# Kernel optimization log

Hardware: AMD Instinct MI355X
Metric: run time of the kernel (lower is better)

## Reference

```python
import jax, jax.numpy as jnp
import numpy as np

H = 8  # num_heads
EPS = 1e-5


def layer_norm(x, g, b):
    mu = jnp.mean(x, axis=-1, keepdims=True)
    var = jnp.mean((x - mu) ** 2, axis=-1, keepdims=True)
    return (x - mu) * jax.lax.rsqrt(var + EPS) * g + b


def setup_inputs() -> dict:
    key = jax.random.key(0)
    ks = jax.random.split(key, 8)
    B, N, C = 2, 2048, 512
    Dff = 2048
    s = 0.02
    x = jax.random.normal(ks[0], (B, N, C), dtype=jnp.float32)
    mask = (jax.random.uniform(ks[1], (N, N)) > 0.5).astype(jnp.float32)
    return {
        "x": x,
        "mask": mask,
        "w_qkv": jax.random.normal(ks[2], (3 * C, C), dtype=jnp.float32) * s,
        "w_proj": jax.random.normal(ks[3], (C, C), dtype=jnp.float32) * s,
        "b_proj": jnp.zeros((C,), jnp.float32),
        "g1": jnp.ones((C,), jnp.float32),
        "beta1": jnp.zeros((C,), jnp.float32),
        "g2": jnp.ones((C,), jnp.float32),
        "beta2": jnp.zeros((C,), jnp.float32),
        "w1": jax.random.normal(ks[4], (Dff, C), dtype=jnp.float32) * s,
        "bm1": jnp.zeros((Dff,), jnp.float32),
        "w2": jax.random.normal(ks[5], (C, Dff), dtype=jnp.float32) * s,
        "bm2": jnp.zeros((C,), jnp.float32),
    }


def attn_block(h, mask, w_qkv, w_proj, b_proj):
    B, N, C = h.shape
    hd = C // H
    scale = hd ** -0.5
    qkv = (h @ w_qkv.T).reshape(B, N, 3, H, hd)
    q, k, v = jnp.moveaxis(qkv, 2, 0)          # each [B, N, H, hd]
    q = q.transpose(0, 2, 1, 3)                 # [B, H, N, hd]
    k = k.transpose(0, 2, 1, 3)
    v = v.transpose(0, 2, 1, 3)
    attn = jnp.einsum("bhnd,bhmd->bhnm", q, k) * scale
    attn = attn * mask                          # multiplicative sparse mask
    attn = jax.nn.softmax(attn, axis=-1)
    o = jnp.einsum("bhnm,bhmd->bhnd", attn, v)
    o = o.transpose(0, 2, 1, 3).reshape(B, N, C)
    return o @ w_proj.T + b_proj


def reference(x, mask, w_qkv, w_proj, b_proj, g1, beta1, g2, beta2, w1, bm1, w2, bm2):
    # pre-norm transformer block, dropout/drop_path disabled (eval)
    y = x + attn_block(layer_norm(x, g1, beta1), mask, w_qkv, w_proj, b_proj)
    h = layer_norm(y, g2, beta2)
    h = jax.nn.gelu(h @ w1.T + bm1, approximate=False)  # torch F.gelu default (erf)
    z = y + (h @ w2.T + bm2)
    return z
```

## Files before the change

### kernel.cpp

```cpp
#include <hip/hip_runtime.h>
#include <cmath>
#include <stdint.h>

#define N_SEQ 2048
#define C_DIM 512
#define BATCH 2
#define NHEAD 8
#define DFF   2048
#define M_ROWS (BATCH * N_SEQ)

typedef unsigned short ushort_t;
typedef __bf16 bf16x8 __attribute__((ext_vector_type(8)));
typedef float  f32x4  __attribute__((ext_vector_type(4)));

__device__ __forceinline__ float bf2f(ushort_t u) {
    union { unsigned int i; float f; } v; v.i = ((unsigned int)u) << 16; return v.f;
}
__device__ __forceinline__ ushort_t f2bf_(float f) {
    union { float f; unsigned int i; } v; v.f = f;
    unsigned int r = v.i + 0x7fffu + ((v.i >> 16) & 1u);
    return (ushort_t)(r >> 16);
}

__device__ __forceinline__ void load_lds16(const ushort_t* g, ushort_t* lds_wave_base) {
    __builtin_amdgcn_global_load_lds(
        (const __attribute__((address_space(1))) void*)g,
        (__attribute__((address_space(3))) void*)lds_wave_base, 16, 0, 0);
}

__global__ void probe_kernel(const unsigned int* __restrict__ g1w, int* __restrict__ flag) {
    if (threadIdx.x == 0 && blockIdx.x == 0)
        *flag = (g1w[0] == 0x3F800000u) ? 1 : 0;
}

__global__ __launch_bounds__(256) void convert_kernel(const int* __restrict__ flag,
        const void* w_qkv, const void* w_proj, const void* w1, const void* w2,
        ushort_t* wq_bf, ushort_t* wp_bf, ushort_t* w1_bf, ushort_t* w2_bf) {
    long e = ((long)blockIdx.x * 256 + threadIdx.x) * 8;
    const void* src; ushort_t* dst; long off;
    if      (e < 786432)  { src = w_qkv; dst = wq_bf;  off = e; }
    else if (e < 1048576) { src = w_proj; dst = wp_bf; off = e - 786432; }
    else if (e < 2097152) { src = w1;    dst = w1_bf;  off = e - 1048576; }
    else                  { src = w2;    dst = w2_bf;  off = e - 2097152; }
    bf16x8 r;
    if (*flag) {
        const float4* q = (const float4*)((const float*)src + off);
        float4 a = q[0], b = q[1];
        r[0]=(__bf16)a.x; r[1]=(__bf16)a.y; r[2]=(__bf16)a.z; r[3]=(__bf16)a.w;
        r[4]=(__bf16)b.x; r[5]=(__bf16)b.y; r[6]=(__bf16)b.z; r[7]=(__bf16)b.w;
    } else {
        r = *(const bf16x8*)((const ushort_t*)src + off);
    }
    *(bf16x8*)(dst + off) = r;
}

template <typename TX, typename TG>
__device__ __forceinline__ void ln_body(const TX* __restrict__ x, const TG* __restrict__ g,
                                        const TG* __restrict__ b, ushort_t* __restrict__ out) {
    int row  = blockIdx.x * 4 + (threadIdx.x >> 6);
    int lane = threadIdx.x & 63;
    const TX* xr = x + (size_t)row * C_DIM + lane * 8;
    float v[8];
    if (sizeof(TX) == 2) {
        bf16x8 t = *(const bf16x8*)xr;
        #pragma unroll
        for (int j = 0; j < 8; ++j) v[j] = (float)t[j];
    } else {
        const float4* q = (const float4*)xr;
        float4 a = q[0], c = q[1];
        v[0]=a.x; v[1]=a.y; v[2]=a.z; v[3]=a.w; v[4]=c.x; v[5]=c.y; v[6]=c.z; v[7]=c.w;
    }
    float s = 0.f, sq = 0.f;
    #pragma unroll
    for (int j = 0; j < 8; ++j) { s += v[j]; sq += v[j] * v[j]; }
    #pragma unroll
    for (int m = 1; m < 64; m <<= 1) { s += __shfl_xor(s, m, 64); sq += __shfl_xor(sq, m, 64); }
    float mean = s * (1.0f / C_DIM);
    float var  = fmaxf(sq * (1.0f / C_DIM) - mean * mean, 0.0f);
    float rs = rsqrtf(var + 1e-5f);
    float gv[8], bv[8];
    const TG* gp = g + lane * 8; const TG* bp = b + lane * 8;
    if (sizeof(TG) == 2) {
        bf16x8 tg = *(const bf16x8*)gp, tb = *(const bf16x8*)bp;
        #pragma unroll
        for (int j = 0; j < 8; ++j) { gv[j] = (float)tg[j]; bv[j] = (float)tb[j]; }
    } else {
        const float4* qg = (const float4*)gp; const float4* qb = (const float4*)bp;
        float4 a=qg[0], c=qg[1], d=qb[0], e=qb[1];
        gv[0]=a.x;gv[1]=a.y;gv[2]=a.z;gv[3]=a.w;gv[4]=c.x;gv[5]=c.y;gv[6]=c.z;gv[7]=c.w;
        bv[0]=d.x;bv[1]=d.y;bv[2]=d.z;bv[3]=d.w;bv[4]=e.x;bv[5]=e.y;bv[6]=e.z;bv[7]=e.w;
    }
    bf16x8 o;
    #pragma unroll
    for (int j = 0; j < 8; ++j) o[j] = (__bf16)((v[j] - mean) * rs * gv[j] + bv[j]);
    *(bf16x8*)(out + (size_t)row * C_DIM + lane * 8) = o;
}

__global__ __launch_bounds__(256) void ln1_kernel(const int* __restrict__ flag, const void* x,
                                                  const void* g, const void* b, ushort_t* out) {
    if (*flag) ln_body<float, float>((const float*)x, (const float*)g, (const float*)b, out);
    else       ln_body<ushort_t, ushort_t>((const ushort_t*)x, (const ushort_t*)g, (const ushort_t*)b, out);
}
__global__ __launch_bounds__(256) void ln2_kernel(const int* __restrict__ flag, const ushort_t* y,
                                                  const void* g, const void* b, ushort_t* out) {
    if (*flag) ln_body<ushort_t, float>(y, (const float*)g, (const float*)b, out);
    else       ln_body<ushort_t, ushort_t>(y, (const ushort_t*)g, (const ushort_t*)b, out);
}

template <int BM, int K, bool HAS_BIAS, int ACT, int RES_MODE, int OUT_MODE>
__global__ __launch_bounds__(256) void gemm_kernel(const int* __restrict__ flag,
        const ushort_t* __restrict__ A, const ushort_t* __restrict__ W,
        const void* __restrict__ bias, const void* __restrict__ res,
        void* __restrict__ Cout, int Nout) {
    constexpr int MT = BM / 32;
    __shared__ __align__(16) ushort_t As[BM * 32];
    __shared__ __align__(16) ushort_t Bs[64 * 32];
    int t = threadIdx.x;
    int wave = t >> 6, lane = t & 63, quad = lane >> 4, l16 = lane & 15;
    int wave_m = wave >> 1, wave_n = wave & 1;
    int row0 = blockIdx.y * BM, col0 = blockIdx.x * 64;

    f32x4 acc[MT][2] = {};
    int arow = t >> 2, kofs = (t & 3) * 8;

    for (int k0 = 0; k0 < K; k0 += 32) {
        load_lds16(A + (size_t)(row0 + arow) * K + k0 + kofs, As + wave * 512);
        if (BM == 128)
            load_lds16(A + (size_t)(row0 + 64 + arow) * K + k0 + kofs, As + 2048 + wave * 512);
        load_lds16(W + (size_t)(col0 + arow) * K + k0 + kofs, Bs + wave * 512);
        __syncthreads();
        bf16x8 af[MT], bfr[2];
        #pragma unroll
        for (int i = 0; i < MT; ++i)
            af[i] = *(const bf16x8*)&As[(wave_m * (BM / 2) + i * 16 + l16) * 32 + quad * 8];
        #pragma unroll
        for (int j = 0; j < 2; ++j)
            bfr[j] = *(const bf16x8*)&Bs[(wave_n * 32 + j * 16 + l16) * 32 + quad * 8];
        #pragma unroll
        for (int i = 0; i < MT; ++i)
            #pragma unroll
            for (int j = 0; j < 2; ++j)
                acc[i][j] = __builtin_amdgcn_mfma_f32_16x16x32_bf16(af[i], bfr[j], acc[i][j], 0, 0, 0);
        __syncthreads();
    }

    int is32 = *flag;
    #pragma unroll
    for (int j = 0; j < 2; ++j) {
        int col = col0 + wave_n * 32 + j * 16 + l16;
        float bv = 0.0f;
        if (HAS_BIAS) bv = is32 ? ((const float*)bias)[col] : bf2f(((const ushort_t*)bias)[col]);
        #pragma unroll
        for (int i = 0; i < MT; ++i) {
            #pragma unroll
            for (int r = 0; r < 4; ++r) {
                int row = row0 + wave_m * (BM / 2) + i * 16 + quad * 4 + r;
                float v = acc[i][j][r] + bv;
                if (ACT == 1) v = 0.5f * v * (1.0f + erff(v * 0.70710678118654752f));
                size_t idx = (size_t)row * Nout + col;
                if (RES_MODE == 1) v += is32 ? ((const float*)res)[idx] : bf2f(((const ushort_t*)res)[idx]);
                if (RES_MODE == 3) v += bf2f(((const ushort_t*)res)[idx]);
                if (OUT_MODE == 0) ((ushort_t*)Cout)[idx] = f2bf_(v);
                else { if (is32) ((float*)Cout)[idx] = v; else ((ushort_t*)Cout)[idx] = f2bf_(v); }
            }
        }
    }
}

__global__ __launch_bounds__(256, 5) void attn_kernel(const int* __restrict__ flag,
        const ushort_t* __restrict__ qkv, const void* __restrict__ mask,
        ushort_t* __restrict__ Opart, float* __restrict__ Lpart) {
    __shared__ __align__(16) ushort_t Ks[64][68];
    __shared__ __align__(16) ushort_t VTs[64][68];
    __shared__ __align__(16) ushort_t Ps[4][16][68];
    int bh = blockIdx.x, b = bh >> 3, h = bh & 7;
    int sp = blockIdx.z;
    int t = threadIdx.x;
    int wave = t >> 6, lane = t & 63, quad = lane >> 4, l16 = lane & 15;
    int row0 = blockIdx.y * 64 + wave * 16;
    int is32 = *flag;

    const ushort_t* base = qkv + (size_t)b * N_SEQ * 1536;
    const ushort_t* qp = base + h * 64;
    const ushort_t* kp = base + 512 + h * 64;
    const ushort_t* vp = base + 1024 + h * 64;
    const float* mask32 = (const float*)mask;
    const ushort_t* mask16 = (const ushort_t*)mask;
    size_t mbase[4];
    #pragma unroll
    for (int r = 0; r < 4; ++r) mbase[r] = (size_t)(row0 + quad * 4 + r) * N_SEQ;

    bf16x8 aq[2];
    #pragma unroll
    for (int c = 0; c < 2; ++c)
        aq[c] = *(const bf16x8*)(qp + (size_t)(row0 + l16) * 1536 + c * 32 + quad * 8);

    f32x4 o_acc[4] = {};
    float lsum[4] = {};
    const float scale = 0.125f;

    int k_key[2], k_d[2], v_key[2], v_db[2];
    #pragma unroll
    for (int s = 0; s < 2; ++s) {
        int e = s * 256 + t;
        k_key[s] = e >> 3;  k_d[s]  = (e & 7) * 8;
        v_key[s] = e & 63;  v_db[s] = (e >> 6) * 8;
    }
    const int n_base = sp * 512;
    bf16x8 kreg[2], vreg[2];
    #pragma unroll
    for (int s = 0; s < 2; ++s) {
        kreg[s] = *(const bf16x8*)(kp + (size_t)(n_base + k_key[s]) * 1536 + k_d[s]);
        vreg[s] = *(const bf16x8*)(vp + (size_t)(n_base + v_key[s]) * 1536 + v_db[s]);
    }
    float mreg[16];
    #pragma unroll
    for (int g = 0; g < 4; ++g)
        #pragma unroll
        for (int r = 0; r < 4; ++r) {
            size_t midx = mbase[r] + n_base + g * 16 + l16;
            mreg[g * 4 + r] = is32 ? mask32[midx] : bf2f(mask16[midx]);
        }

    for (int i = 0; i < 8; ++i) {
        int n0 = n_base + i * 64;
        __syncthreads();
        #pragma unroll
        for (int s = 0; s < 2; ++s)
            *(bf16x8*)&Ks[k_key[s]][k_d[s]] = kreg[s];
        #pragma unroll
        for (int s = 0; s < 2; ++s)
            #pragma unroll
            for (int j = 0; j < 8; ++j)
                VTs[v_db[s] + j][v_key[s]] = __builtin_bit_cast(unsigned short, vreg[s][j]);
        __syncthreads();
        if (i < 7) {
            int n1 = n0 + 64;
            #pragma unroll
            for (int s = 0; s < 2; ++s) {
                kreg[s] = *(const bf16x8*)(kp + (size_t)(n1 + k_key[s]) * 1536 + k_d[s]);
                vreg[s] = *(const bf16x8*)(vp + (size_t)(n1 + v_key[s]) * 1536 + v_db[s]);
            }
        }
        f32x4 s_acc[4] = {};
        #pragma unroll
        for (int g = 0; g < 4; ++g)
            #pragma unroll
            for (int c = 0; c < 2; ++c) {
                bf16x8 bk = *(const bf16x8*)&Ks[g * 16 + l16][c * 32 + quad * 8];
                s_acc[g] = __builtin_amdgcn_mfma_f32_16x16x32_bf16(aq[c], bk, s_acc[g], 0, 0, 0);
            }
        #pragma unroll
        for (int g = 0; g < 4; ++g)
            #pragma unroll
            for (int r = 0; r < 4; ++r) {
                float p = __expf(s_acc[g][r] * scale * mreg[g * 4 + r]);
                lsum[r] += p;
                Ps[wave][quad * 4 + r][g * 16 + l16] = __builtin_bit_cast(unsigned short, (__bf16)p);
            }
        if (i < 7) {
            #pragma unroll
            for (int g = 0; g < 4; ++g)
                #pragma unroll
                for (int r = 0; r < 4; ++r) {
                    size_t midx = mbase[r] + n0 + 64 + g * 16 + l16;
                    mreg[g * 4 + r] = is32 ? mask32[midx] : bf2f(mask16[midx]);
                }
        }
        bf16x8 pf[2];
        #pragma unroll
        for (int c = 0; c < 2; ++c)
            pf[c] = *(const bf16x8*)&Ps[wave][l16][c * 32 + quad * 8];
        #pragma unroll
        for (int d = 0; d < 4; ++d)
            #pragma unroll
            for (int c = 0; c < 2; ++c) {
                bf16x8 bv = *(const bf16x8*)&VTs[d * 16 + l16][c * 32 + quad * 8];
                o_acc[d] = __builtin_amdgcn_mfma_f32_16x16x32_bf16(pf[c], bv, o_acc[d], 0, 0, 0);
            }
    }
    #pragma unroll
    for (int m = 1; m < 16; m <<= 1)
        #pragma unroll
        for (int r = 0; r < 4; ++r) lsum[r] += __shfl_xor(lsum[r], m, 64);
    ushort_t* op = Opart + (size_t)(sp * 16 + bh) * N_SEQ * 64;
    #pragma unroll
    for (int r = 0; r < 4; ++r) {
        int row = row0 + quad * 4 + r;
        #pragma unroll
        for (int d = 0; d < 4; ++d)
            op[(size_t)row * 64 + d * 16 + l16] = f2bf_(o_acc[d][r]);
    }
    if (l16 == 0) {
        #pragma unroll
        for (int r = 0; r < 4; ++r)
            Lpart[(size_t)(sp * 16 + bh) * N_SEQ + row0 + quad * 4 + r] = lsum[r];
    }
}

__global__ __launch_bounds__(256) void combine_kernel(const ushort_t* __restrict__ Opart,
        const float* __restrict__ Lpart, ushort_t* __restrict__ attno) {
    int gid = blockIdx.x * 256 + threadIdx.x;
    int rowg = gid >> 4;
    int dq = (gid & 15) * 4;
    int bh = rowg >> 11, q = rowg & 2047, b = bh >> 3, h = bh & 7;
    const size_t SP = (size_t)16 * N_SEQ * 64;
    float acc[4] = {};
    float l = 0.0f;
    #pragma unroll
    for (int sp = 0; sp < 4; ++sp) {
        ushort4 o = *(const ushort4*)&Opart[sp * SP + (size_t)rowg * 64 + dq];
        acc[0] += bf2f(o.x); acc[1] += bf2f(o.y); acc[2] += bf2f(o.z); acc[3] += bf2f(o.w);
        l += Lpart[(size_t)sp * 16 * N_SEQ + rowg];
    }
    float inv = 1.0f / l;
    ushort4 res;
    res.x = f2bf_(acc[0] * inv); res.y = f2bf_(acc[1] * inv);
    res.z = f2bf_(acc[2] * inv); res.w = f2bf_(acc[3] * inv);
    *(ushort4*)&attno[((size_t)b * N_SEQ + q) * C_DIM + h * 64 + dq] = res;
}

extern "C" void kernel_launch(void* const* d_in, const int* in_sizes, int n_in,
                              void* d_out, int out_size, void* d_ws, size_t ws_size,
                              hipStream_t stream) {
    char* ws = (char*)d_ws;
    const size_t KB = 1024;
    int*      flag  = (int*)ws;
    ushort_t* wq_bf = (ushort_t*)(ws + 256 * KB);
    ushort_t* wp_bf = (ushort_t*)(ws + 1792 * KB);
    ushort_t* w1_bf = (ushort_t*)(ws + 2304 * KB);
    ushort_t* w2_bf = (ushort_t*)(ws + 4352 * KB);
    ushort_t* h     = (ushort_t*)(ws + 6400 * KB);
    ushort_t* attno = (ushort_t*)(ws + 6400 * KB);
    ushort_t* qkv   = (ushort_t*)(ws + 10496 * KB);
    ushort_t* Opart = (ushort_t*)(ws + 22784 * KB);
    float*    Lpart = (float*)   (ws + 39168 * KB);
    ushort_t* y     = (ushort_t*)(ws + 35072 * KB);
    ushort_t* gmid  = (ushort_t*)(ws + 10496 * KB);

    probe_kernel<<<1, 64, 0, stream>>>((const unsigned int*)d_in[5], flag);
    convert_kernel<<<1536, 256, 0, stream>>>(flag, d_in[2], d_in[3], d_in[9], d_in[11],
                                             wq_bf, wp_bf, w1_bf, w2_bf);
    ln1_kernel<<<M_ROWS / 4, 256, 0, stream>>>(flag, d_in[0], d_in[5], d_in[6], h);
    gemm_kernel<128, 512, false, 0, 0, 0><<<dim3(1536 / 64, 32), 256, 0, stream>>>(
        flag, h, wq_bf, nullptr, nullptr, qkv, 1536);
    attn_kernel<<<dim3(BATCH * NHEAD, N_SEQ / 64, 4), 256, 0, stream>>>(flag, qkv, d_in[1], Opart, Lpart);
    combine_kernel<<<2048, 256, 0, stream>>>(Opart, Lpart, attno);
    gemm_kernel<64, 512, true, 0, 1, 0><<<dim3(C_DIM / 64, 64), 256, 0, stream>>>(
        flag, attno, wp_bf, d_in[4], d_in[0], y, C_DIM);
    ln2_kernel<<<M_ROWS / 4, 256, 0, stream>>>(flag, y, d_in[7], d_in[8], h);
    gemm_kernel<128, 512, true, 1, 0, 0><<<dim3(DFF / 64, 32), 256, 0, stream>>>(
        flag, h, w1_bf, d_in[10], nullptr, gmid, DFF);
    gemm_kernel<64, 2048, true, 0, 3, 2><<<dim3(C_DIM / 64, 64), 256, 0, stream>>>(
        flag, gmid, w2_bf, d_in[12], y, d_out, C_DIM);
}
```

Before: 275.9 us.

## Pack mask to bits, switch attention to 32x32 MFMA, double GEMM k-step

```diff
diff --git a/kernel.cpp b/kernel.cpp
--- a/kernel.cpp
+++ b/kernel.cpp
@@ -10,8 +10,10 @@
 #define M_ROWS (BATCH * N_SEQ)
 
 typedef unsigned short ushort_t;
+typedef unsigned long long u64;
 typedef __bf16 bf16x8 __attribute__((ext_vector_type(8)));
 typedef float  f32x4  __attribute__((ext_vector_type(4)));
+typedef float  f32x16 __attribute__((ext_vector_type(16)));
 
 __device__ __forceinline__ float bf2f(ushort_t u) {
     union { unsigned int i; float f; } v; v.i = ((unsigned int)u) << 16; return v.f;
@@ -54,6 +56,20 @@
     *(bf16x8*)(dst + off) = r;
 }
 
+__global__ __launch_bounds__(256) void maskpack_kernel(const int* __restrict__ flag,
+        const void* __restrict__ mask, u64* __restrict__ maskT) {
+    int key = blockIdx.x * 256 + threadIdx.x;
+    int qw  = blockIdx.y;
+    int is32 = *flag;
+    u64 bits = 0;
+    for (int j = 0; j < 64; ++j) {
+        bool m = is32 ? (((const float*)mask)[(size_t)(qw * 64 + j) * N_SEQ + key] != 0.0f)
+                      : ((((const ushort_t*)mask)[(size_t)(qw * 64 + j) * N_SEQ + key] & 0x7fffu) != 0);
+        bits |= (u64)m << j;
+    }
+    maskT[(size_t)key * 32 + qw] = bits;
+}
+
 template <typename TX, typename TG>
 __device__ __forceinline__ void ln_body(const TX* __restrict__ x, const TG* __restrict__ g,
                                         const TG* __restrict__ b, ushort_t* __restrict__ out) {
@@ -113,8 +129,8 @@
         const void* __restrict__ bias, const void* __restrict__ res,
         void* __restrict__ Cout, int Nout) {
     constexpr int MT = BM / 32;
-    __shared__ __align__(16) ushort_t As[BM * 32];
-    __shared__ __align__(16) ushort_t Bs[64 * 32];
+    __shared__ __align__(16) ushort_t As[2][BM][32];
+    __shared__ __align__(16) ushort_t Bs[2][64][32];
     int t = threadIdx.x;
     int wave = t >> 6, lane = t & 63, quad = lane >> 4, l16 = lane & 15;
     int wave_m = wave >> 1, wave_n = wave & 1;
@@ -123,24 +139,30 @@
     f32x4 acc[MT][2] = {};
     int arow = t >> 2, kofs = (t & 3) * 8;
 
-    for (int k0 = 0; k0 < K; k0 += 32) {
-        load_lds16(A + (size_t)(row0 + arow) * K + k0 + kofs, As + wave * 512);
-        if (BM == 128)
-            load_lds16(A + (size_t)(row0 + 64 + arow) * K + k0 + kofs, As + 2048 + wave * 512);
-        load_lds16(W + (size_t)(col0 + arow) * K + k0 + kofs, Bs + wave * 512);
+    for (int k0 = 0; k0 < K; k0 += 64) {
+        #pragma unroll
+        for (int h = 0; h < 2; ++h) {
+            load_lds16(A + (size_t)(row0 + arow) * K + k0 + h * 32 + kofs, &As[h][0][0] + wave * 512);
+            if (BM == 128)
+                load_lds16(A + (size_t)(row0 + 64 + arow) * K + k0 + h * 32 + kofs, &As[h][64][0] + wave * 512);
+            load_lds16(W + (size_t)(col0 + arow) * K + k0 + h * 32 + kofs, &Bs[h][0][0] + wave * 512);
+        }
         __syncthreads();
-        bf16x8 af[MT], bfr[2];
-        #pragma unroll
-        for (int i = 0; i < MT; ++i)
-            af[i] = *(const bf16x8*)&As[(wave_m * (BM / 2) + i * 16 + l16) * 32 + quad * 8];
-        #pragma unroll
-        for (int j = 0; j < 2; ++j)
-            bfr[j] = *(const bf16x8*)&Bs[(wave_n * 32 + j * 16 + l16) * 32 + quad * 8];
-        #pragma unroll
-        for (int i = 0; i < MT; ++i)
+        #pragma unroll
+        for (int h = 0; h < 2; ++h) {
+            bf16x8 af[MT], bfr[2];
+            #pragma unroll
+            for (int i = 0; i < MT; ++i)
+                af[i] = *(const bf16x8*)&As[h][wave_m * (BM / 2) + i * 16 + l16][quad * 8];
             #pragma unroll
             for (int j = 0; j < 2; ++j)
-                acc[i][j] = __builtin_amdgcn_mfma_f32_16x16x32_bf16(af[i], bfr[j], acc[i][j], 0, 0, 0);
+                bfr[j] = *(const bf16x8*)&Bs[h][wave_n * 32 + j * 16 + l16][quad * 8];
+            #pragma unroll
+            for (int i = 0; i < MT; ++i)
+                #pragma unroll
+                for (int j = 0; j < 2; ++j)
+                    acc[i][j] = __builtin_amdgcn_mfma_f32_16x16x32_bf16(af[i], bfr[j], acc[i][j], 0, 0, 0);
+        }
         __syncthreads();
     }
 
@@ -167,134 +189,125 @@
     }
 }
 
-__global__ __launch_bounds__(256, 5) void attn_kernel(const int* __restrict__ flag,
-        const ushort_t* __restrict__ qkv, const void* __restrict__ mask,
+__global__ __launch_bounds__(128, 3) void attn_kernel(const int* __restrict__ flag,
+        const ushort_t* __restrict__ qkv, const u64* __restrict__ maskT,
         ushort_t* __restrict__ Opart, float* __restrict__ Lpart) {
-    __shared__ __align__(16) ushort_t Ks[64][68];
+    __shared__ __align__(16) ushort_t Ks[64][64];
     __shared__ __align__(16) ushort_t VTs[64][68];
-    __shared__ __align__(16) ushort_t Ps[4][16][68];
-    int bh = blockIdx.x, b = bh >> 3, h = bh & 7;
-    int sp = blockIdx.z;
+    __shared__ __align__(16) ushort_t Ps[2][32][68];
     int t = threadIdx.x;
-    int wave = t >> 6, lane = t & 63, quad = lane >> 4, l16 = lane & 15;
-    int row0 = blockIdx.y * 64 + wave * 16;
-    int is32 = *flag;
+    int wave = t >> 6, lane = t & 63, l32 = lane & 31, half = lane >> 5;
+    int qtile = blockIdx.x, bh = blockIdx.y, sp = blockIdx.z;
+    int b = bh >> 3, h = bh & 7;
+    int qbase = qtile * 64;
 
     const ushort_t* base = qkv + (size_t)b * N_SEQ * 1536;
     const ushort_t* qp = base + h * 64;
     const ushort_t* kp = base + 512 + h * 64;
     const ushort_t* vp = base + 1024 + h * 64;
-    const float* mask32 = (const float*)mask;
-    const ushort_t* mask16 = (const ushort_t*)mask;
-    size_t mbase[4];
-    #pragma unroll
-    for (int r = 0; r < 4; ++r) mbase[r] = (size_t)(row0 + quad * 4 + r) * N_SEQ;
-
-    bf16x8 aq[2];
-    #pragma unroll
-    for (int c = 0; c < 2; ++c)
-        aq[c] = *(const bf16x8*)(qp + (size_t)(row0 + l16) * 1536 + c * 32 + quad * 8);
-
-    f32x4 o_acc[4] = {};
-    float lsum[4] = {};
+
+    bf16x8 aq[4];
+    int qrow = qbase + wave * 32 + l32;
+    #pragma unroll
+    for (int c = 0; c < 4; ++c)
+        aq[c] = *(const bf16x8*)(qp + (size_t)qrow * 1536 + c * 16 + half * 8);
+
+    f32x16 o_acc[2] = {};
+    float lsum[16] = {};
     const float scale = 0.125f;
 
-    int k_key[2], k_d[2], v_key[2], v_db[2];
+    int v_kp[2], v_db[2];
     #pragma unroll
     for (int s = 0; s < 2; ++s) {
-        int e = s * 256 + t;
-        k_key[s] = e >> 3;  k_d[s]  = (e & 7) * 8;
-        v_key[s] = e & 63;  v_db[s] = (e >> 6) * 8;
+        int idx = s * 128 + t;
+        v_kp[s] = (idx & 31) * 2;
+        v_db[s] = (idx >> 5) * 8;
     }
     const int n_base = sp * 512;
-    bf16x8 kreg[2], vreg[2];
-    #pragma unroll
-    for (int s = 0; s < 2; ++s) {
-        kreg[s] = *(const bf16x8*)(kp + (size_t)(n_base + k_key[s]) * 1536 + k_d[s]);
-        vreg[s] = *(const bf16x8*)(vp + (size_t)(n_base + v_key[s]) * 1536 + v_db[s]);
-    }
-    float mreg[16];
-    #pragma unroll
-    for (int g = 0; g < 4; ++g)
-        #pragma unroll
-        for (int r = 0; r < 4; ++r) {
-            size_t midx = mbase[r] + n_base + g * 16 + l16;
-            mreg[g * 4 + r] = is32 ? mask32[midx] : bf2f(mask16[midx]);
-        }
+    bf16x8 vreg[2][2];
+    #pragma unroll
+    for (int s = 0; s < 2; ++s)
+        #pragma unroll
+        for (int u = 0; u < 2; ++u)
+            vreg[s][u] = *(const bf16x8*)(vp + (size_t)(n_base + v_kp[s] + u) * 1536 + v_db[s]);
+    u64 mw[2];
+    #pragma unroll
+    for (int t2 = 0; t2 < 2; ++t2)
+        mw[t2] = maskT[(size_t)(n_base + t2 * 32 + l32) * 32 + qtile];
 
     for (int i = 0; i < 8; ++i) {
         int n0 = n_base + i * 64;
         __syncthreads();
         #pragma unroll
+        for (int s = 0; s < 4; ++s)
+            load_lds16(kp + (size_t)(n0 + (s * 2 + wave) * 8 + (lane >> 3)) * 1536 + (lane & 7) * 8,
+                       &Ks[(s * 2 + wave) * 8][0]);
+        #pragma unroll
         for (int s = 0; s < 2; ++s)
-            *(bf16x8*)&Ks[k_key[s]][k_d[s]] = kreg[s];
-        #pragma unroll
-        for (int s = 0; s < 2; ++s)
-            #pragma unroll
-            for (int j = 0; j < 8; ++j)
-                VTs[v_db[s] + j][v_key[s]] = __builtin_bit_cast(unsigned short, vreg[s][j]);
+            #pragma unroll
+            for (int j = 0; j < 8; ++j) {
+                unsigned int pair = (unsigned int)__builtin_bit_cast(unsigned short, vreg[s][0][j])
+                                  | ((unsigned int)__builtin_bit_cast(unsigned short, vreg[s][1][j]) << 16);
+                *(unsigned int*)&VTs[v_db[s] + j][v_kp[s]] = pair;
+            }
         __syncthreads();
         if (i < 7) {
             int n1 = n0 + 64;
             #pragma unroll
-            for (int s = 0; s < 2; ++s) {
-                kreg[s] = *(const bf16x8*)(kp + (size_t)(n1 + k_key[s]) * 1536 + k_d[s]);
-                vreg[s] = *(const bf16x8*)(vp + (size_t)(n1 + v_key[s]) * 1536 + v_db[s]);
-            }
-        }
-        f32x4 s_acc[4] = {};
-        #pragma unroll
-        for (int g = 0; g < 4; ++g)
-            #pragma unroll
-            for (int c = 0; c < 2; ++c) {
-                bf16x8 bk = *(const bf16x8*)&Ks[g * 16 + l16][c * 32 + quad * 8];
-                s_acc[g] = __builtin_amdgcn_mfma_f32_16x16x32_bf16(aq[c], bk, s_acc[g], 0, 0, 0);
-            }
-        #pragma unroll
-        for (int g = 0; g < 4; ++g)
-            #pragma unroll
-            for (int r = 0; r < 4; ++r) {
-                float p = __expf(s_acc[g][r] * scale * mreg[g * 4 + r]);
+            for (int s = 0; s < 2; ++s)
+                #pragma unroll
+                for (int u = 0; u < 2; ++u)
+                    vreg[s][u] = *(const bf16x8*)(vp + (size_t)(n1 + v_kp[s] + u) * 1536 + v_db[s]);
+        }
+        f32x16 s_acc[2] = {};
+        #pragma unroll
+        for (int t2 = 0; t2 < 2; ++t2)
+            #pragma unroll
+            for (int c = 0; c < 4; ++c) {
+                bf16x8 bk = *(const bf16x8*)&Ks[t2 * 32 + l32][c * 16 + half * 8];
+                s_acc[t2] = __builtin_amdgcn_mfma_f32_32x32x16_bf16(aq[c], bk, s_acc[t2], 0, 0, 0);
+            }
+        #pragma unroll
+        for (int t2 = 0; t2 < 2; ++t2)
+            #pragma unroll
+            for (int r = 0; r < 16; ++r) {
+                int row_local = (r & 3) + 8 * (r >> 2) + 4 * half;
+                float e = __expf(s_acc[t2][r] * scale);
+                float p = ((mw[t2] >> (wave * 32 + row_local)) & 1) ? e : 1.0f;
                 lsum[r] += p;
-                Ps[wave][quad * 4 + r][g * 16 + l16] = __builtin_bit_cast(unsigned short, (__bf16)p);
+                Ps[wave][row_local][t2 * 32 + l32] = __builtin_bit_cast(unsigned short, (__bf16)p);
             }
         if (i < 7) {
             #pragma unroll
-            for (int g = 0; g < 4; ++g)
-                #pragma unroll
-                for (int r = 0; r < 4; ++r) {
-                    size_t midx = mbase[r] + n0 + 64 + g * 16 + l16;
-                    mreg[g * 4 + r] = is32 ? mask32[midx] : bf2f(mask16[midx]);
-                }
-        }
-        bf16x8 pf[2];
-        #pragma unroll
-        for (int c = 0; c < 2; ++c)
-            pf[c] = *(const bf16x8*)&Ps[wave][l16][c * 32 + quad * 8];
-        #pragma unroll
-        for (int d = 0; d < 4; ++d)
-            #pragma unroll
-            for (int c = 0; c < 2; ++c) {
-                bf16x8 bv = *(const bf16x8*)&VTs[d * 16 + l16][c * 32 + quad * 8];
-                o_acc[d] = __builtin_amdgcn_mfma_f32_16x16x32_bf16(pf[c], bv, o_acc[d], 0, 0, 0);
-            }
-    }
-    #pragma unroll
-    for (int m = 1; m < 16; m <<= 1)
-        #pragma unroll
-        for (int r = 0; r < 4; ++r) lsum[r] += __shfl_xor(lsum[r], m, 64);
+            for (int t2 = 0; t2 < 2; ++t2)
+                mw[t2] = maskT[(size_t)(n0 + 64 + t2 * 32 + l32) * 32 + qtile];
+        }
+        bf16x8 pf[4];
+        #pragma unroll
+        for (int kc = 0; kc < 4; ++kc)
+            pf[kc] = *(const bf16x8*)&Ps[wave][l32][kc * 16 + half * 8];
+        #pragma unroll
+        for (int dt = 0; dt < 2; ++dt)
+            #pragma unroll
+            for (int kc = 0; kc < 4; ++kc) {
+                bf16x8 bv = *(const bf16x8*)&VTs[dt * 32 + l32][kc * 16 + half * 8];
+                o_acc[dt] = __builtin_amdgcn_mfma_f32_32x32x16_bf16(pf[kc], bv, o_acc[dt], 0, 0, 0);
+            }
+    }
+    #pragma unroll
+    for (int m = 1; m < 32; m <<= 1)
+        #pragma unroll
+        for (int r = 0; r < 16; ++r) lsum[r] += __shfl_xor(lsum[r], m, 64);
     ushort_t* op = Opart + (size_t)(sp * 16 + bh) * N_SEQ * 64;
     #pragma unroll
-    for (int r = 0; r < 4; ++r) {
-        int row = row0 + quad * 4 + r;
-        #pragma unroll
-        for (int d = 0; d < 4; ++d)
-            op[(size_t)row * 64 + d * 16 + l16] = f2bf_(o_acc[d][r]);
-    }
-    if (l16 == 0) {
-        #pragma unroll
-        for (int r = 0; r < 4; ++r)
-            Lpart[(size_t)(sp * 16 + bh) * N_SEQ + row0 + quad * 4 + r] = lsum[r];
+    for (int r = 0; r < 16; ++r) {
+        int row_local = (r & 3) + 8 * (r >> 2) + 4 * half;
+        int q = qbase + wave * 32 + row_local;
+        #pragma unroll
+        for (int dt = 0; dt < 2; ++dt)
+            op[(size_t)q * 64 + dt * 32 + l32] = f2bf_(o_acc[dt][r]);
+        if (l32 == 0)
+            Lpart[(size_t)(sp * 16 + bh) * N_SEQ + q] = lsum[r];
     }
 }
 
@@ -330,21 +343,23 @@
     ushort_t* wp_bf = (ushort_t*)(ws + 1792 * KB);
     ushort_t* w1_bf = (ushort_t*)(ws + 2304 * KB);
     ushort_t* w2_bf = (ushort_t*)(ws + 4352 * KB);
-    ushort_t* h     = (ushort_t*)(ws + 6400 * KB);
-    ushort_t* attno = (ushort_t*)(ws + 6400 * KB);
-    ushort_t* qkv   = (ushort_t*)(ws + 10496 * KB);
-    ushort_t* Opart = (ushort_t*)(ws + 22784 * KB);
-    float*    Lpart = (float*)   (ws + 39168 * KB);
-    ushort_t* y     = (ushort_t*)(ws + 35072 * KB);
-    ushort_t* gmid  = (ushort_t*)(ws + 10496 * KB);
+    u64*      maskT = (u64*)     (ws + 6400 * KB);
+    ushort_t* h     = (ushort_t*)(ws + 6912 * KB);
+    ushort_t* attno = (ushort_t*)(ws + 11008 * KB);
+    ushort_t* qkv   = (ushort_t*)(ws + 15104 * KB);
+    ushort_t* Opart = (ushort_t*)(ws + 27392 * KB);
+    float*    Lpart = (float*)   (ws + 43776 * KB);
+    ushort_t* y     = (ushort_t*)(ws + 27392 * KB);
+    ushort_t* gmid  = (ushort_t*)(ws + 11008 * KB);
 
     probe_kernel<<<1, 64, 0, stream>>>((const unsigned int*)d_in[5], flag);
     convert_kernel<<<1536, 256, 0, stream>>>(flag, d_in[2], d_in[3], d_in[9], d_in[11],
                                              wq_bf, wp_bf, w1_bf, w2_bf);
+    maskpack_kernel<<<dim3(8, 32), 256, 0, stream>>>(flag, d_in[1], maskT);
     ln1_kernel<<<M_ROWS / 4, 256, 0, stream>>>(flag, d_in[0], d_in[5], d_in[6], h);
     gemm_kernel<128, 512, false, 0, 0, 0><<<dim3(1536 / 64, 32), 256, 0, stream>>>(
         flag, h, wq_bf, nullptr, nullptr, qkv, 1536);
-    attn_kernel<<<dim3(BATCH * NHEAD, N_SEQ / 64, 4), 256, 0, stream>>>(flag, qkv, d_in[1], Opart, Lpart);
+    attn_kernel<<<dim3(N_SEQ / 64, BATCH * NHEAD, 4), 128, 0, stream>>>(flag, qkv, maskT, Opart, Lpart);
     combine_kernel<<<2048, 256, 0, stream>>>(Opart, Lpart, attno);
     gemm_kernel<64, 512, true, 0, 1, 0><<<dim3(C_DIM / 64, 64), 256, 0, stream>>>(
         flag, attno, wp_bf, d_in[4], d_in[0], y, C_DIM);
```

Result: slower. 295.7 us (+7.2%).
